# Optimization experiments

Hardware: AMD Instinct MI355X
Metric: run time of the kernel (lower is better)

## Reference

```python
import jax, jax.numpy as jnp
import numpy as np

N = 50000
E = 800000
IN_DIM = 128
OUT_DIM = 128


def setup_inputs() -> dict:
    key = jax.random.key(0)
    k1, k2, k3, k4 = jax.random.split(key, 4)
    x = jax.random.normal(k1, (N, IN_DIM), dtype=jnp.float32)
    edge_index = jax.random.randint(k2, (2, E), 0, N, dtype=jnp.int64)
    # Linear(in_dim*2, out_dim) params
    W = jax.random.normal(k3, (2 * IN_DIM, OUT_DIM), dtype=jnp.float32) * (1.0 / np.sqrt(2 * IN_DIM))
    b = jax.random.normal(k4, (OUT_DIM,), dtype=jnp.float32) * 0.01
    return {"x": x, "edge_index": edge_index, "W": W, "b": b}


def reference(x, edge_index, W, b):
    src, dst = edge_index[0], edge_index[1]
    diff = x[src] - x[dst]                              # (E, C)
    # segment-max over destination nodes; empty segments get -inf identity
    seg_max = jax.ops.segment_max(diff, dst, num_segments=N)  # (N, C)
    counts = jax.ops.segment_sum(jnp.ones((E,), dtype=jnp.int32), dst, num_segments=N)
    # original code leaves zeros for nodes with no incoming edges
    max_diff = jnp.where((counts > 0)[:, None], seg_max, jnp.zeros_like(seg_max))
    x_cat = jnp.concatenate([x, max_diff], axis=-1)     # (N, 2C)
    return x_cat @ W + b
```

## Files before the change

### kernel.cpp

```cpp
#include <hip/hip_runtime.h>
#include <math.h>

#define NN 50000
#define NE 800000
#define CD 128
#define NBKT 49
#define CAP 24576
#define SLICE 4096
#define EBLK 196
#define CASTB 2048
#define NBLK2 1563
#define SUBCAP 768

typedef __attribute__((ext_vector_type(8))) short short8;
typedef __attribute__((ext_vector_type(4))) float f32x4;


__device__ inline unsigned pack2bf(float lo, float hi) {
    unsigned a = __float_as_uint(lo), b = __float_as_uint(hi);
    a = (a + 0x7fffu + ((a >> 16) & 1u)) >> 16;
    b = (b + 0x7fffu + ((b >> 16) & 1u)) & 0xffff0000u;
    return a | b;
}

__device__ inline unsigned short f2bf(float f) {
    unsigned u = __float_as_uint(f);
    return (unsigned short)((u + 0x7fffu + ((u >> 16) & 1u)) >> 16);
}

__device__ inline void fmax2(float& a, float& b, unsigned v) {
    a = fmaxf(a, __uint_as_float(v << 16));
    b = fmaxf(b, __uint_as_float(v & 0xffff0000u));
}


__global__ __launch_bounds__(256) void prep5_k(const int* __restrict__ ei,
                                               const float* __restrict__ x,
                                               const float* __restrict__ W,
                                               int* __restrict__ cur,
                                               int* __restrict__ ovfn,
                                               unsigned* __restrict__ ovf,
                                               unsigned* __restrict__ csr,
                                               unsigned* __restrict__ xb,
                                               unsigned short* __restrict__ wt) {
    int b = blockIdx.x;
    int t = threadIdx.x;
    if (b < EBLK) {
        __shared__ int hist[64];
        __shared__ int curs[64];
        int e0 = b * SLICE;
        int e1 = min(NE, e0 + SLICE);
        if (t < 64) hist[t] = 0;
        __syncthreads();
        for (int e = e0 + t; e < e1; e += 256)
            atomicAdd(&hist[((unsigned)ei[NE + e]) >> 10], 1);
        __syncthreads();
        if (t < NBKT) curs[t] = atomicAdd(&cur[t], hist[t]);
        __syncthreads();
        for (int e = e0 + t; e < e1; e += 256) {
            int d = ei[NE + e];
            int s = ei[e];
            int bin = ((unsigned)d) >> 10;
            int p = atomicAdd(&curs[bin], 1);
            if (p < CAP) {
                csr[(size_t)bin * CAP + p] = ((unsigned)s << 10) | (unsigned)(d & 1023);
            } else {
                int op = atomicAdd(ovfn, 1);
                ovf[op] = ((unsigned)s << 16) | (unsigned)d;
            }
        }
    } else {
        int tid0 = (b - EBLK) * 256 + t;
        for (int i = tid0; i < NN * CD / 4; i += CASTB * 256) {
            float4 v = ((const float4*)x)[i];
            uint2 r;
            r.x = pack2bf(v.x, v.y);
            r.y = pack2bf(v.z, v.w);
            ((uint2*)xb)[i] = r;
        }
        for (int i = tid0; i < 2 * CD * CD; i += CASTB * 256) {
            int n = i >> 8, k = i & 255;
            wt[(size_t)n * 256 + k] = f2bf(W[(size_t)k * 128 + n]);
        }
    }
}


__global__ __launch_bounds__(256) void rebin_k(const int* __restrict__ cur,
                                               const unsigned* __restrict__ csr,
                                               int* __restrict__ subcur,
                                               int* __restrict__ ovfn2,
                                               unsigned* __restrict__ ovf2,
                                               unsigned* __restrict__ csr2) {
    __shared__ int hist[32];
    __shared__ int curs[32];
    int b = blockIdx.x, t = threadIdx.x;
    int q = b >> 3, s = b & 7;
    int cnt = min(cur[q], CAP);
    int i0 = (cnt * s) >> 3, i1 = (cnt * (s + 1)) >> 3;
    if (t < 32) hist[t] = 0;
    __syncthreads();
    const unsigned* base = csr + (size_t)q * CAP;
    for (int i = i0 + t; i < i1; i += 256)
        atomicAdd(&hist[(base[i] >> 5) & 31], 1);
    __syncthreads();
    if (t < 32) curs[t] = atomicAdd(&subcur[q * 32 + t], hist[t]);
    __syncthreads();
    for (int i = i0 + t; i < i1; i += 256) {
        unsigned w = base[i];
        int sub = (int)((w >> 5) & 31u);
        int p = atomicAdd(&curs[sub], 1);
        if (p < SUBCAP) {
            csr2[(size_t)(q * 32 + sub) * SUBCAP + p] = ((w >> 10) << 5) | (w & 31u);
        } else {
            int op = atomicAdd(ovfn2, 1);
            ovf2[op] = ((w >> 10) << 16) | (unsigned)(q * 1024 + (int)(w & 1023u));
        }
    }
}


__global__ __launch_bounds__(256) void fused_k(const unsigned* __restrict__ xb,
                                               const int* __restrict__ subcur,
                                               const int* __restrict__ ovfn,
                                               const unsigned* __restrict__ ovf,
                                               const int* __restrict__ ovfn2,
                                               const unsigned* __restrict__ ovf2,
                                               const unsigned* __restrict__ csr2,
                                               const short* __restrict__ wt,
                                               const float* __restrict__ bias,
                                               float* __restrict__ out) {
    __shared__ unsigned short idx[32][72];
    __shared__ unsigned short amx[32][136];
    __shared__ int lcnt[32];
    __shared__ int spill[512];
    __shared__ int spn;

    int t = threadIdx.x;
    int B = blockIdx.x;
    int nbase = B * 32;

    if (t < 32) lcnt[t] = 0;
    if (t == 32) spn = 0;
    __syncthreads();

    int cnt = min(subcur[B], SUBCAP);
    const unsigned* base = csr2 + (size_t)B * SUBCAP;
    for (int i = t; i < cnt; i += 256) {
        unsigned w = base[i];
        int ln = (int)(w & 31u);
        int s = (int)(w >> 5);
        int pos = atomicAdd(&lcnt[ln], 1);
        if (pos < 64) idx[ln][pos] = (unsigned short)s;
        else { int sp = atomicAdd(&spn, 1); if (sp < 512) spill[sp] = (s << 6) | ln; }
    }
    int ovN = min(ovfn[0], NE);
    for (int i = t; i < ovN; i += 256) {
        unsigned w = ovf[i];
        int d = (int)(w & 0xffffu);
        if ((d >> 5) == B) {
            int ln = d & 31;
            int s = (int)(w >> 16);
            int pos = atomicAdd(&lcnt[ln], 1);
            if (pos < 64) idx[ln][pos] = (unsigned short)s;
            else { int sp = atomicAdd(&spn, 1); if (sp < 512) spill[sp] = (s << 6) | ln; }
        }
    }
    int ovN2 = min(ovfn2[0], NE);
    for (int i = t; i < ovN2; i += 256) {
        unsigned w = ovf2[i];
        int d = (int)(w & 0xffffu);
        if ((d >> 5) == B) {
            int ln = d & 31;
            int s = (int)(w >> 16);
            int pos = atomicAdd(&lcnt[ln], 1);
            if (pos < 64) idx[ln][pos] = (unsigned short)s;
            else { int sp = atomicAdd(&spn, 1); if (sp < 512) spill[sp] = (s << 6) | ln; }
        }
    }
    __syncthreads();

    int w = t >> 6, lane = t & 63;
    int q4 = lane >> 4, c = lane & 15;
    int sN = min(spn, 512);
#pragma unroll 1
    for (int cb = 0; cb < 4; cb++) {
        const unsigned* xcb = xb + cb * 16 + c;
#pragma unroll 1
        for (int j = 0; j < 2; j++) {
            int ln = w * 8 + j * 4 + q4;
            int node = nbase + ln;
            int lc = lcnt[ln];
            int lim = min(lc, 64);
            float m0 = -INFINITY, m1 = -INFINITY;

            for (int bb = 0; bb < lim; bb += 8) {
                uint4 pk = *(const uint4*)&idx[ln][bb];
                int s0 = (int)(pk.x & 0xffffu), s1 = (int)(pk.x >> 16);
                int s2 = (int)(pk.y & 0xffffu), s3 = (int)(pk.y >> 16);
                int s4 = (int)(pk.z & 0xffffu), s5 = (int)(pk.z >> 16);
                int s6 = (int)(pk.w & 0xffffu), s7 = (int)(pk.w >> 16);
                if (bb + 8 <= lim) {
                    unsigned v0 = xcb[(size_t)s0 * 64];
                    unsigned v1 = xcb[(size_t)s1 * 64];
                    unsigned v2 = xcb[(size_t)s2 * 64];
                    unsigned v3 = xcb[(size_t)s3 * 64];
                    unsigned v4 = xcb[(size_t)s4 * 64];
                    unsigned v5 = xcb[(size_t)s5 * 64];
                    unsigned v6 = xcb[(size_t)s6 * 64];
                    unsigned v7 = xcb[(size_t)s7 * 64];
                    fmax2(m0, m1, v0); fmax2(m0, m1, v1);
                    fmax2(m0, m1, v2); fmax2(m0, m1, v3);
                    fmax2(m0, m1, v4); fmax2(m0, m1, v5);
                    fmax2(m0, m1, v6); fmax2(m0, m1, v7);
                } else {
                    if (bb + 0 < lim) fmax2(m0, m1, xcb[(size_t)s0 * 64]);
                    if (bb + 1 < lim) fmax2(m0, m1, xcb[(size_t)s1 * 64]);
                    if (bb + 2 < lim) fmax2(m0, m1, xcb[(size_t)s2 * 64]);
                    if (bb + 3 < lim) fmax2(m0, m1, xcb[(size_t)s3 * 64]);
                    if (bb + 4 < lim) fmax2(m0, m1, xcb[(size_t)s4 * 64]);
                    if (bb + 5 < lim) fmax2(m0, m1, xcb[(size_t)s5 * 64]);
                    if (bb + 6 < lim) fmax2(m0, m1, xcb[(size_t)s6 * 64]);
                    if (bb + 7 < lim) fmax2(m0, m1, xcb[(size_t)s7 * 64]);
                }
            }
            for (int i = 0; i < sN; i++) {
                int sw = spill[i];
                if ((sw & 63) == ln) fmax2(m0, m1, xcb[(size_t)(sw >> 6) * 64]);
            }
            unsigned r = 0u;
            if (lc > 0) {
                unsigned xd = xcb[(size_t)node * 64];
                float d0 = m0 - __uint_as_float(xd << 16);
                float d1 = m1 - __uint_as_float(xd & 0xffff0000u);
                r = pack2bf(d0, d1);
            }
            *(unsigned*)&amx[ln][cb * 32 + c * 2] = r;
        }
    }
    __syncthreads();

    int mm = lane & 15, g4 = lane >> 4;
    int rt = w & 1, ch = w >> 1;
    int r0 = nbase + rt * 16;
    int row = r0 + mm;
    bool rowok = row < NN;

    f32x4 acc[4];
#pragma unroll
    for (int ct = 0; ct < 4; ct++) {
        float bv = bias[ch * 64 + ct * 16 + mm];
        acc[ct] = (f32x4){bv, bv, bv, bv};
    }

    const short* xbs = (const short*)xb;
#pragma unroll
    for (int kc = 0; kc < 8; kc++) {
        int k0 = kc * 32;
        short8 a;
        if (kc < 4) {
            a = (short8){0, 0, 0, 0, 0, 0, 0, 0};
            if (rowok) a = *(const short8*)(xbs + (size_t)row * 128 + k0 + g4 * 8);
        } else {
            a = *(const short8*)&amx[rt * 16 + mm][(k0 - 128) + g4 * 8];
        }
#pragma unroll
        for (int ct = 0; ct < 4; ct++) {
            short8 bb = *(const short8*)(wt + (size_t)(ch * 64 + ct * 16 + mm) * 256 + k0 + g4 * 8);
            acc[ct] = __builtin_amdgcn_mfma_f32_16x16x32_bf16(a, bb, acc[ct], 0, 0, 0);
        }
    }

#pragma unroll
    for (int ct = 0; ct < 4; ct++) {
#pragma unroll
        for (int i = 0; i < 4; i++) {
            int rr = r0 + g4 * 4 + i;
            if (rr < NN) out[(size_t)rr * 128 + ch * 64 + ct * 16 + mm] = acc[ct][i];
        }
    }
}


extern "C" void kernel_launch(void* const* d_in, const int* in_sizes, int n_in,
                              void* d_out, int out_size, void* d_ws, size_t ws_size,
                              hipStream_t stream) {
    const float* x = (const float*)d_in[0];
    const int* ei = (const int*)d_in[1];
    const float* W = (const float*)d_in[2];
    const float* bias = (const float*)d_in[3];
    float* out = (float*)d_out;

    int* wsi = (int*)d_ws;
    int* cur    = wsi;
    int* ovfn   = wsi + 64;
    int* subcur = wsi + 80;
    int* ovfn2  = wsi + 1648;
    unsigned* ovf  = (unsigned*)(wsi + 2048);
    unsigned* csr  = (unsigned*)(wsi + 802048);
    unsigned* csr2 = (unsigned*)(wsi + 2006272);
    unsigned* ovf2 = (unsigned*)(wsi + 3210496);
    unsigned* xb   = (unsigned*)(wsi + 4010496);
    unsigned short* wt = (unsigned short*)(wsi + 7210496);

    hipMemsetAsync(cur, 0, 2048 * sizeof(int), stream);

    prep5_k<<<EBLK + CASTB, 256, 0, stream>>>(ei, x, W, cur, ovfn, ovf, csr, xb, wt);
    rebin_k<<<NBKT * 8, 256, 0, stream>>>(cur, csr, subcur, ovfn2, ovf2, csr2);
    fused_k<<<NBLK2, 256, 0, stream>>>(xb, subcur, ovfn, ovf, ovfn2, ovf2, csr2,
                                       (const short*)wt, bias, out);
}
```

Before: 199.9 us.

## Split fused gather-GEMM into channel-sliced gather and separate GEMM kernels

Stores the bf16 copy of x in four channel-sliced planes so each gather block touches a 64-byte row slice. The gather now runs as four times as many blocks, one per channel slice, and writes fp32 max-diffs into the output buffer. A separate GEMM kernel reads those back, converts them to bf16 and overwrites the output with the linear layer result. It also merges the two overflow lists, caps their size, and shrinks the bucket capacities. The aim is better cache locality and more parallelism in the gather, at the cost of an extra kernel launch and an fp32 round trip of the max-diff tensor through global memory.

```diff
diff --git a/kernel.cpp b/kernel.cpp
--- a/kernel.cpp
+++ b/kernel.cpp
@@ -5,12 +5,14 @@
 #define NE 800000
 #define CD 128
 #define NBKT 49
-#define CAP 24576
+#define CAP 17152
 #define SLICE 4096
 #define EBLK 196
 #define CASTB 2048
 #define NBLK2 1563
-#define SUBCAP 768
+#define SUBCAP 640
+#define OVFCAP 65536
+#define SSTR 800000
 
 typedef __attribute__((ext_vector_type(8))) short short8;
 typedef __attribute__((ext_vector_type(4))) float f32x4;
@@ -66,17 +68,18 @@
                 csr[(size_t)bin * CAP + p] = ((unsigned)s << 10) | (unsigned)(d & 1023);
             } else {
                 int op = atomicAdd(ovfn, 1);
-                ovf[op] = ((unsigned)s << 16) | (unsigned)d;
+                if (op < OVFCAP) ovf[op] = ((unsigned)s << 16) | (unsigned)d;
             }
         }
     } else {
         int tid0 = (b - EBLK) * 256 + t;
         for (int i = tid0; i < NN * CD / 4; i += CASTB * 256) {
             float4 v = ((const float4*)x)[i];
+            int n = i >> 5, f = i & 31;
             uint2 r;
             r.x = pack2bf(v.x, v.y);
             r.y = pack2bf(v.z, v.w);
-            ((uint2*)xb)[i] = r;
+            *(uint2*)(xb + (size_t)(f >> 3) * SSTR + n * 16 + (f & 7) * 2) = r;
         }
         for (int i = tid0; i < 2 * CD * CD; i += CASTB * 256) {
             int n = i >> 8, k = i & 255;
@@ -89,8 +92,8 @@
 __global__ __launch_bounds__(256) void rebin_k(const int* __restrict__ cur,
                                                const unsigned* __restrict__ csr,
                                                int* __restrict__ subcur,
-                                               int* __restrict__ ovfn2,
-                                               unsigned* __restrict__ ovf2,
+                                               int* __restrict__ ovfn,
+                                               unsigned* __restrict__ ovf,
                                                unsigned* __restrict__ csr2) {
     __shared__ int hist[32];
     __shared__ int curs[32];
@@ -113,31 +116,28 @@
         if (p < SUBCAP) {
             csr2[(size_t)(q * 32 + sub) * SUBCAP + p] = ((w >> 10) << 5) | (w & 31u);
         } else {
-            int op = atomicAdd(ovfn2, 1);
-            ovf2[op] = ((w >> 10) << 16) | (unsigned)(q * 1024 + (int)(w & 1023u));
-        }
-    }
-}
-
-
-__global__ __launch_bounds__(256) void fused_k(const unsigned* __restrict__ xb,
-                                               const int* __restrict__ subcur,
-                                               const int* __restrict__ ovfn,
-                                               const unsigned* __restrict__ ovf,
-                                               const int* __restrict__ ovfn2,
-                                               const unsigned* __restrict__ ovf2,
-                                               const unsigned* __restrict__ csr2,
-                                               const short* __restrict__ wt,
-                                               const float* __restrict__ bias,
-                                               float* __restrict__ out) {
+            int op = atomicAdd(ovfn, 1);
+            if (op < OVFCAP) ovf[op] = ((w >> 10) << 16) | (unsigned)(q * 1024 + (int)(w & 1023u));
+        }
+    }
+}
+
+
+__global__ __launch_bounds__(256) void gather_k(const unsigned* __restrict__ xb,
+                                                const int* __restrict__ subcur,
+                                                const int* __restrict__ ovfn,
+                                                const unsigned* __restrict__ ovf,
+                                                const unsigned* __restrict__ csr2,
+                                                float* __restrict__ out) {
     __shared__ unsigned short idx[32][72];
-    __shared__ unsigned short amx[32][136];
     __shared__ int lcnt[32];
     __shared__ int spill[512];
     __shared__ int spn;
 
     int t = threadIdx.x;
-    int B = blockIdx.x;
+    int bid = blockIdx.x;
+    int cb = bid / NBLK2;
+    int B = bid - cb * NBLK2;
     int nbase = B * 32;
 
     if (t < 32) lcnt[t] = 0;
@@ -154,7 +154,7 @@
         if (pos < 64) idx[ln][pos] = (unsigned short)s;
         else { int sp = atomicAdd(&spn, 1); if (sp < 512) spill[sp] = (s << 6) | ln; }
     }
-    int ovN = min(ovfn[0], NE);
+    int ovN = min(ovfn[0], OVFCAP);
     for (int i = t; i < ovN; i += 256) {
         unsigned w = ovf[i];
         int d = (int)(w & 0xffffu);
@@ -166,117 +166,115 @@
             else { int sp = atomicAdd(&spn, 1); if (sp < 512) spill[sp] = (s << 6) | ln; }
         }
     }
-    int ovN2 = min(ovfn2[0], NE);
-    for (int i = t; i < ovN2; i += 256) {
-        unsigned w = ovf2[i];
-        int d = (int)(w & 0xffffu);
-        if ((d >> 5) == B) {
-            int ln = d & 31;
-            int s = (int)(w >> 16);
-            int pos = atomicAdd(&lcnt[ln], 1);
-            if (pos < 64) idx[ln][pos] = (unsigned short)s;
-            else { int sp = atomicAdd(&spn, 1); if (sp < 512) spill[sp] = (s << 6) | ln; }
-        }
-    }
-    __syncthreads();
-
-    int w = t >> 6, lane = t & 63;
+    __syncthreads();
+
+    int w4 = t >> 6, lane = t & 63;
     int q4 = lane >> 4, c = lane & 15;
+    const unsigned* xs = xb + (size_t)cb * SSTR + c;
     int sN = min(spn, 512);
 #pragma unroll 1
-    for (int cb = 0; cb < 4; cb++) {
-        const unsigned* xcb = xb + cb * 16 + c;
-#pragma unroll 1
-        for (int j = 0; j < 2; j++) {
-            int ln = w * 8 + j * 4 + q4;
-            int node = nbase + ln;
-            int lc = lcnt[ln];
-            int lim = min(lc, 64);
-            float m0 = -INFINITY, m1 = -INFINITY;
-
-            for (int bb = 0; bb < lim; bb += 8) {
-                uint4 pk = *(const uint4*)&idx[ln][bb];
-                int s0 = (int)(pk.x & 0xffffu), s1 = (int)(pk.x >> 16);
-                int s2 = (int)(pk.y & 0xffffu), s3 = (int)(pk.y >> 16);
-                int s4 = (int)(pk.z & 0xffffu), s5 = (int)(pk.z >> 16);
-                int s6 = (int)(pk.w & 0xffffu), s7 = (int)(pk.w >> 16);
-                if (bb + 8 <= lim) {
-                    unsigned v0 = xcb[(size_t)s0 * 64];
-                    unsigned v1 = xcb[(size_t)s1 * 64];
-                    unsigned v2 = xcb[(size_t)s2 * 64];
-                    unsigned v3 = xcb[(size_t)s3 * 64];
-                    unsigned v4 = xcb[(size_t)s4 * 64];
-                    unsigned v5 = xcb[(size_t)s5 * 64];
-                    unsigned v6 = xcb[(size_t)s6 * 64];
-                    unsigned v7 = xcb[(size_t)s7 * 64];
-                    fmax2(m0, m1, v0); fmax2(m0, m1, v1);
-                    fmax2(m0, m1, v2); fmax2(m0, m1, v3);
-                    fmax2(m0, m1, v4); fmax2(m0, m1, v5);
-                    fmax2(m0, m1, v6); fmax2(m0, m1, v7);
-                } else {
-                    if (bb + 0 < lim) fmax2(m0, m1, xcb[(size_t)s0 * 64]);
-                    if (bb + 1 < lim) fmax2(m0, m1, xcb[(size_t)s1 * 64]);
-                    if (bb + 2 < lim) fmax2(m0, m1, xcb[(size_t)s2 * 64]);
-                    if (bb + 3 < lim) fmax2(m0, m1, xcb[(size_t)s3 * 64]);
-                    if (bb + 4 < lim) fmax2(m0, m1, xcb[(size_t)s4 * 64]);
-                    if (bb + 5 < lim) fmax2(m0, m1, xcb[(size_t)s5 * 64]);
-                    if (bb + 6 < lim) fmax2(m0, m1, xcb[(size_t)s6 * 64]);
-                    if (bb + 7 < lim) fmax2(m0, m1, xcb[(size_t)s7 * 64]);
-                }
+    for (int j = 0; j < 2; j++) {
+        int ln = w4 * 8 + j * 4 + q4;
+        int node = nbase + ln;
+        int lc = lcnt[ln];
+        int lim = min(lc, 64);
+        float m0 = -INFINITY, m1 = -INFINITY;
+
+        for (int bb = 0; bb < lim; bb += 8) {
+            uint4 pk = *(const uint4*)&idx[ln][bb];
+            int s0 = (int)(pk.x & 0xffffu), s1 = (int)(pk.x >> 16);
+            int s2 = (int)(pk.y & 0xffffu), s3 = (int)(pk.y >> 16);
+            int s4 = (int)(pk.z & 0xffffu), s5 = (int)(pk.z >> 16);
+            int s6 = (int)(pk.w & 0xffffu), s7 = (int)(pk.w >> 16);
+            if (bb + 8 <= lim) {
+                unsigned v0 = xs[(size_t)s0 * 16];
+                unsigned v1 = xs[(size_t)s1 * 16];
+                unsigned v2 = xs[(size_t)s2 * 16];
+                unsigned v3 = xs[(size_t)s3 * 16];
+                unsigned v4 = xs[(size_t)s4 * 16];
+                unsigned v5 = xs[(size_t)s5 * 16];
+                unsigned v6 = xs[(size_t)s6 * 16];
+                unsigned v7 = xs[(size_t)s7 * 16];
+                fmax2(m0, m1, v0); fmax2(m0, m1, v1);
+                fmax2(m0, m1, v2); fmax2(m0, m1, v3);
+                fmax2(m0, m1, v4); fmax2(m0, m1, v5);
+                fmax2(m0, m1, v6); fmax2(m0, m1, v7);
+            } else {
+                if (bb + 0 < lim) fmax2(m0, m1, xs[(size_t)s0 * 16]);
+                if (bb + 1 < lim) fmax2(m0, m1, xs[(size_t)s1 * 16]);
+                if (bb + 2 < lim) fmax2(m0, m1, xs[(size_t)s2 * 16]);
+                if (bb + 3 < lim) fmax2(m0, m1, xs[(size_t)s3 * 16]);
+                if (bb + 4 < lim) fmax2(m0, m1, xs[(size_t)s4 * 16]);
+                if (bb + 5 < lim) fmax2(m0, m1, xs[(size_t)s5 * 16]);
+                if (bb + 6 < lim) fmax2(m0, m1, xs[(size_t)s6 * 16]);
+                if (bb + 7 < lim) fmax2(m0, m1, xs[(size_t)s7 * 16]);
             }
-            for (int i = 0; i < sN; i++) {
-                int sw = spill[i];
-                if ((sw & 63) == ln) fmax2(m0, m1, xcb[(size_t)(sw >> 6) * 64]);
+        }
+        for (int i = 0; i < sN; i++) {
+            int sw = spill[i];
+            if ((sw & 63) == ln) fmax2(m0, m1, xs[(size_t)(sw >> 6) * 16]);
+        }
+        if (node < NN) {
+            float2 r = make_float2(0.f, 0.f);
+            if (lc > 0) {
+                unsigned xd = xs[(size_t)node * 16];
+                r.x = m0 - __uint_as_float(xd << 16);
+                r.y = m1 - __uint_as_float(xd & 0xffff0000u);
             }
-            unsigned r = 0u;
-            if (lc > 0) {
-                unsigned xd = xcb[(size_t)node * 64];
-                float d0 = m0 - __uint_as_float(xd << 16);
-                float d1 = m1 - __uint_as_float(xd & 0xffff0000u);
-                r = pack2bf(d0, d1);
-            }
-            *(unsigned*)&amx[ln][cb * 32 + c * 2] = r;
-        }
-    }
-    __syncthreads();
-
-    int mm = lane & 15, g4 = lane >> 4;
-    int rt = w & 1, ch = w >> 1;
-    int r0 = nbase + rt * 16;
-    int row = r0 + mm;
+            *(float2*)(out + (size_t)node * 128 + cb * 32 + c * 2) = r;
+        }
+    }
+}
+
+
+__global__ __launch_bounds__(256) void gemm_k(const unsigned* __restrict__ xb,
+                                              const short* __restrict__ wt,
+                                              const float* __restrict__ bias,
+                                              float* __restrict__ out) {
+    int t = threadIdx.x;
+    int w = t >> 6, lane = t & 63;
+    int m = lane & 15, g = lane >> 4;
+    int r0 = blockIdx.x * 64 + w * 16;
+    int row = r0 + m;
     bool rowok = row < NN;
 
-    f32x4 acc[4];
-#pragma unroll
-    for (int ct = 0; ct < 4; ct++) {
-        float bv = bias[ch * 64 + ct * 16 + mm];
+    f32x4 acc[8];
+#pragma unroll
+    for (int ct = 0; ct < 8; ct++) {
+        float bv = bias[ct * 16 + m];
         acc[ct] = (f32x4){bv, bv, bv, bv};
     }
 
-    const short* xbs = (const short*)xb;
 #pragma unroll
     for (int kc = 0; kc < 8; kc++) {
         int k0 = kc * 32;
-        short8 a;
-        if (kc < 4) {
-            a = (short8){0, 0, 0, 0, 0, 0, 0, 0};
-            if (rowok) a = *(const short8*)(xbs + (size_t)row * 128 + k0 + g4 * 8);
-        } else {
-            a = *(const short8*)&amx[rt * 16 + mm][(k0 - 128) + g4 * 8];
-        }
-#pragma unroll
-        for (int ct = 0; ct < 4; ct++) {
-            short8 bb = *(const short8*)(wt + (size_t)(ch * 64 + ct * 16 + mm) * 256 + k0 + g4 * 8);
-            acc[ct] = __builtin_amdgcn_mfma_f32_16x16x32_bf16(a, bb, acc[ct], 0, 0, 0);
-        }
-    }
-
-#pragma unroll
-    for (int ct = 0; ct < 4; ct++) {
+        short8 a = (short8){0, 0, 0, 0, 0, 0, 0, 0};
+        if (rowok) {
+            if (kc < 4) {
+                a = *(const short8*)(xb + (size_t)kc * SSTR + (size_t)row * 16 + g * 4);
+            } else {
+                const float* p = out + (size_t)row * 128 + (k0 - 128) + g * 8;
+                float4 u = *(const float4*)p;
+                float4 v = *(const float4*)(p + 4);
+                a = (short8){(short)f2bf(u.x), (short)f2bf(u.y), (short)f2bf(u.z), (short)f2bf(u.w),
+                             (short)f2bf(v.x), (short)f2bf(v.y), (short)f2bf(v.z), (short)f2bf(v.w)};
+            }
+        }
+#pragma unroll
+        for (int ct = 0; ct < 8; ct++) {
+            short8 b = *(const short8*)(wt + (size_t)(ct * 16 + m) * 256 + k0 + g * 8);
+            acc[ct] = __builtin_amdgcn_mfma_f32_16x16x32_bf16(a, b, acc[ct], 0, 0, 0);
+        }
+    }
+
+    __syncthreads();
+
+#pragma unroll
+    for (int ct = 0; ct < 8; ct++) {
 #pragma unroll
         for (int i = 0; i < 4; i++) {
-            int rr = r0 + g4 * 4 + i;
-            if (rr < NN) out[(size_t)rr * 128 + ch * 64 + ct * 16 + mm] = acc[ct][i];
+            int rr = r0 + g * 4 + i;
+            if (rr < NN) out[(size_t)rr * 128 + ct * 16 + m] = acc[ct][i];
         }
     }
 }
@@ -295,18 +293,16 @@
     int* cur    = wsi;
     int* ovfn   = wsi + 64;
     int* subcur = wsi + 80;
-    int* ovfn2  = wsi + 1648;
     unsigned* ovf  = (unsigned*)(wsi + 2048);
-    unsigned* csr  = (unsigned*)(wsi + 802048);
-    unsigned* csr2 = (unsigned*)(wsi + 2006272);
-    unsigned* ovf2 = (unsigned*)(wsi + 3210496);
-    unsigned* xb   = (unsigned*)(wsi + 4010496);
-    unsigned short* wt = (unsigned short*)(wsi + 7210496);
+    unsigned* csr  = (unsigned*)(wsi + 67584);
+    unsigned* csr2 = (unsigned*)(wsi + 908032);
+    unsigned* xb   = (unsigned*)(wsi + 1911552);
+    unsigned short* wt = (unsigned short*)(wsi + 5111552);
 
     hipMemsetAsync(cur, 0, 2048 * sizeof(int), stream);
 
     prep5_k<<<EBLK + CASTB, 256, 0, stream>>>(ei, x, W, cur, ovfn, ovf, csr, xb, wt);
-    rebin_k<<<NBKT * 8, 256, 0, stream>>>(cur, csr, subcur, ovfn2, ovf2, csr2);
-    fused_k<<<NBLK2, 256, 0, stream>>>(xb, subcur, ovfn, ovf, ovfn2, ovf2, csr2,
-                                       (const short*)wt, bias, out);
-}
+    rebin_k<<<NBKT * 8, 256, 0, stream>>>(cur, csr, subcur, ovfn, ovf, csr2);
+    gather_k<<<NBLK2 * 4, 256, 0, stream>>>(xb, subcur, ovfn, ovf, csr2, out);
+    gemm_k<<<(NN + 63) / 64, 256, 0, stream>>>(xb, (const short*)wt, bias, out);
+}
```

Result: faster. 188.9 us (-5.5%).
